# Kernel tuning notes

Measured on AMD Instinct MI355X. Metric: run time of the kernel, lower is better.

## Reference

```python
import jax, jax.numpy as jnp
import numpy as np

# Pyramid of RBS (Givens) gates on 6 wires: 15 gates, column-major diamond order.
PYRAMID_PAIRS = [(0,1),(1,2),(0,1),(2,3),(1,2),(3,4),(0,1),(2,3),(4,5),(1,2),(3,4),(0,1),(2,3),(1,2),(0,1)]


def setup_inputs() -> dict:
    key = jax.random.key(0)
    k1, k2, k3, k4, k5, k6 = jax.random.split(key, 6)
    B = 65536
    return {
        "inputs": jax.random.normal(k1, (B, 28, 28), dtype=jnp.float32),
        "dense_w": jax.random.normal(k2, (784, 6), dtype=jnp.float32) * 0.05,
        "dense_b": jax.random.normal(k3, (6,), dtype=jnp.float32) * 0.05,
        # module initializes quantum_weights to zeros; use small random angles for a
        # non-degenerate reference (zeros makes the pyramid the identity)
        "qweights": jax.random.normal(k4, (15,), dtype=jnp.float32) * 0.1,
        "out_w": jax.random.normal(k5, (6, 1), dtype=jnp.float32) * 0.5,
        "out_b": jax.random.normal(k6, (1,), dtype=jnp.float32) * 0.1,
    }


def _quantum_block(h, qweights):
    # vector_loader: encode normalized h into unary amplitudes (Hamming-weight-1 subspace)
    a = h / jnp.linalg.norm(h, axis=1, keepdims=True)  # [B, 6]; NaN if zero norm, sanitized below
    # pyramid_circuit: each RBS(theta) acts as a 2x2 Givens rotation on unary amplitudes
    for k, (i, j) in enumerate(PYRAMID_PAIRS):
        c, s = jnp.cos(qweights[k]), jnp.sin(qweights[k])
        ai, aj = a[:, i], a[:, j]
        a = a.at[:, i].set(c * ai + s * aj)
        a = a.at[:, j].set(-s * ai + c * aj)
    # <Z_i> on a unary state = 1 - 2 * P(qubit i = 1) = 1 - 2 * a_i^2
    z = 1.0 - 2.0 * a * a
    return jnp.where(jnp.isnan(z), jnp.zeros_like(z), z)


def reference(inputs, dense_w, dense_b, qweights, out_w, out_b):
    x = inputs.reshape(inputs.shape[0], -1)          # flatten [B, 784]
    h = x @ dense_w + dense_b                        # Dense(6, linear)
    z = _quantum_block(h, qweights)                  # batched statevector sim, [B, 6]
    return jax.nn.sigmoid(z @ out_w + out_b)         # Dense(1, sigmoid)
```

## Files before the change

### kernel.cpp

```cpp
#include <hip/hip_runtime.h>
#include <math.h>

#define TPB 256

__global__ __launch_bounds__(TPB) void hybrid_kernel(
    const float* __restrict__ inp,
    const float* __restrict__ dw,
    const float* __restrict__ db,
    const float* __restrict__ qw,
    const float* __restrict__ ow,
    const float* __restrict__ ob,
    float* __restrict__ out,
    int B)
{
    __shared__ float4 wT4[6 * 196];
    __shared__ float csc[15], css[15];
    __shared__ float sb[8], sw[8];
    __shared__ float sob;

    float* wT = (float*)wT4;
    const int tid = threadIdx.x;

    for (int i = tid; i < 4704; i += TPB) {
        int e = i / 6;
        int j = i - e * 6;
        wT[j * 784 + e] = dw[i];
    }
    if (tid < 15) { float q = qw[tid]; csc[tid] = cosf(q); css[tid] = sinf(q); }
    if (tid < 6)  { sb[tid] = db[tid]; sw[tid] = ow[tid]; }
    if (tid == 0) sob = ob[0];
    __syncthreads();

    const int lane = tid & 63;
    const int grp  = lane >> 4;
    const int gl   = lane & 15;
    const int row  = blockIdx.x * 16 + (tid >> 6) * 4 + grp;
    if (row >= B) return;

    const float4* x4 = (const float4*)(inp + (size_t)row * 784);

    float acc[6] = {0.f, 0.f, 0.f, 0.f, 0.f, 0.f};

    #pragma unroll 4
    for (int t = 0; t < 12; ++t) {
        const int idx4 = gl + 16 * t;
        const float4 xv = x4[idx4];
        #pragma unroll
        for (int j = 0; j < 6; ++j) {
            const float4 wv = wT4[j * 196 + idx4];
            acc[j] += xv.x * wv.x + xv.y * wv.y + xv.z * wv.z + xv.w * wv.w;
        }
    }
    if (gl < 4) {
        const int idx4 = 192 + gl;
        const float4 xv = x4[idx4];
        #pragma unroll
        for (int j = 0; j < 6; ++j) {
            const float4 wv = wT4[j * 196 + idx4];
            acc[j] += xv.x * wv.x + xv.y * wv.y + xv.z * wv.z + xv.w * wv.w;
        }
    }

    #pragma unroll
    for (int m = 1; m <= 8; m <<= 1) {
        #pragma unroll
        for (int j = 0; j < 6; ++j)
            acc[j] += __shfl_xor(acc[j], m, 64);
    }

    float a[6];
    float hh = 0.f;
    #pragma unroll
    for (int j = 0; j < 6; ++j) {
        a[j] = acc[j] + sb[j];
        hh += a[j] * a[j];
    }
    const float inv = rsqrtf(hh);
    #pragma unroll
    for (int j = 0; j < 6; ++j) a[j] *= inv;

    const int PI[15] = {0,1,0,2,1,3,0,2,4,1,3,0,2,1,0};
    #pragma unroll
    for (int k = 0; k < 15; ++k) {
        const int i = PI[k];
        const float c = csc[k], s = css[k];
        const float ai = a[i], aj = a[i + 1];
        a[i]     = c * ai + s * aj;
        a[i + 1] = c * aj - s * ai;
    }

    float v = sob;
    #pragma unroll
    for (int j = 0; j < 6; ++j) {
        float z = 1.f - 2.f * a[j] * a[j];
        z = isnan(z) ? 0.f : z;
        v += z * sw[j];
    }
    const float o = 1.f / (1.f + __expf(-v));

    if (gl == 0) out[row] = o;
}

extern "C" void kernel_launch(void* const* d_in, const int* in_sizes, int n_in,
                              void* d_out, int out_size, void* d_ws, size_t ws_size,
                              hipStream_t stream) {
    const float* inp = (const float*)d_in[0];
    const float* dw  = (const float*)d_in[1];
    const float* db  = (const float*)d_in[2];
    const float* qw  = (const float*)d_in[3];
    const float* ow  = (const float*)d_in[4];
    const float* ob  = (const float*)d_in[5];
    float* out = (float*)d_out;

    const int B = in_sizes[0] / 784;
    const int blocks = (B + 15) / 16;
    hybrid_kernel<<<blocks, TPB, 0, stream>>>(inp, dw, db, qw, ow, ob, out, B);
}
```

Before: 293.3 us.

## Process four rows per lane group to reuse LDS weights and amortize staging

Result: no change. 298.5 us (+1.8%).

```diff
diff --git a/kernel.cpp b/kernel.cpp
--- a/kernel.cpp
+++ b/kernel.cpp
@@ -34,71 +34,93 @@
     const int lane = tid & 63;
     const int grp  = lane >> 4;
     const int gl   = lane & 15;
-    const int row  = blockIdx.x * 16 + (tid >> 6) * 4 + grp;
-    if (row >= B) return;
+    const int wave = tid >> 6;
+    const int base = blockIdx.x * 64 + wave * 16 + grp * 4;
+    if (base >= B) return;
 
-    const float4* x4 = (const float4*)(inp + (size_t)row * 784);
+    const float4* x0 = (const float4*)(inp + (size_t)base * 784);
 
-    float acc[6] = {0.f, 0.f, 0.f, 0.f, 0.f, 0.f};
+    float acc[4][6];
+    #pragma unroll
+    for (int r = 0; r < 4; ++r)
+        #pragma unroll
+        for (int j = 0; j < 6; ++j) acc[r][j] = 0.f;
 
     #pragma unroll 4
     for (int t = 0; t < 12; ++t) {
         const int idx4 = gl + 16 * t;
-        const float4 xv = x4[idx4];
+        float4 xv[4];
+        #pragma unroll
+        for (int r = 0; r < 4; ++r) xv[r] = x0[r * 196 + idx4];
         #pragma unroll
         for (int j = 0; j < 6; ++j) {
             const float4 wv = wT4[j * 196 + idx4];
-            acc[j] += xv.x * wv.x + xv.y * wv.y + xv.z * wv.z + xv.w * wv.w;
+            #pragma unroll
+            for (int r = 0; r < 4; ++r)
+                acc[r][j] += xv[r].x * wv.x + xv[r].y * wv.y
+                           + xv[r].z * wv.z + xv[r].w * wv.w;
         }
     }
     if (gl < 4) {
         const int idx4 = 192 + gl;
-        const float4 xv = x4[idx4];
+        float4 xv[4];
+        #pragma unroll
+        for (int r = 0; r < 4; ++r) xv[r] = x0[r * 196 + idx4];
         #pragma unroll
         for (int j = 0; j < 6; ++j) {
             const float4 wv = wT4[j * 196 + idx4];
-            acc[j] += xv.x * wv.x + xv.y * wv.y + xv.z * wv.z + xv.w * wv.w;
+            #pragma unroll
+            for (int r = 0; r < 4; ++r)
+                acc[r][j] += xv[r].x * wv.x + xv[r].y * wv.y
+                           + xv[r].z * wv.z + xv[r].w * wv.w;
         }
     }
 
     #pragma unroll
     for (int m = 1; m <= 8; m <<= 1) {
         #pragma unroll
-        for (int j = 0; j < 6; ++j)
-            acc[j] += __shfl_xor(acc[j], m, 64);
+        for (int r = 0; r < 4; ++r)
+            #pragma unroll
+            for (int j = 0; j < 6; ++j)
+                acc[r][j] += __shfl_xor(acc[r][j], m, 64);
     }
 
-    float a[6];
-    float hh = 0.f;
+    const int PI[15] = {0,1,0,2,1,3,0,2,4,1,3,0,2,1,0};
+    float4 o4;
+    float* op = (float*)&o4;
     #pragma unroll
-    for (int j = 0; j < 6; ++j) {
-        a[j] = acc[j] + sb[j];
-        hh += a[j] * a[j];
-    }
-    const float inv = rsqrtf(hh);
-    #pragma unroll
-    for (int j = 0; j < 6; ++j) a[j] *= inv;
+    for (int r = 0; r < 4; ++r) {
+        float a[6];
+        float hh = 0.f;
+        #pragma unroll
+        for (int j = 0; j < 6; ++j) {
+            a[j] = acc[r][j] + sb[j];
+            hh += a[j] * a[j];
+        }
+        const float inv = rsqrtf(hh);
+        #pragma unroll
+        for (int j = 0; j < 6; ++j) a[j] *= inv;
 
-    const int PI[15] = {0,1,0,2,1,3,0,2,4,1,3,0,2,1,0};
-    #pragma unroll
-    for (int k = 0; k < 15; ++k) {
-        const int i = PI[k];
-        const float c = csc[k], s = css[k];
-        const float ai = a[i], aj = a[i + 1];
-        a[i]     = c * ai + s * aj;
-        a[i + 1] = c * aj - s * ai;
+        #pragma unroll
+        for (int k = 0; k < 15; ++k) {
+            const int i = PI[k];
+            const float c = csc[k], s = css[k];
+            const float ai = a[i], aj = a[i + 1];
+            a[i]     = c * ai + s * aj;
+            a[i + 1] = c * aj - s * ai;
+        }
+
+        float v = sob;
+        #pragma unroll
+        for (int j = 0; j < 6; ++j) {
+            float z = 1.f - 2.f * a[j] * a[j];
+            z = isnan(z) ? 0.f : z;
+            v += z * sw[j];
+        }
+        op[r] = 1.f / (1.f + __expf(-v));
     }
 
-    float v = sob;
-    #pragma unroll
-    for (int j = 0; j < 6; ++j) {
-        float z = 1.f - 2.f * a[j] * a[j];
-        z = isnan(z) ? 0.f : z;
-        v += z * sw[j];
-    }
-    const float o = 1.f / (1.f + __expf(-v));
-
-    if (gl == 0) out[row] = o;
+    if (gl == 0) *(float4*)(out + base) = o4;
 }
 
 extern "C" void kernel_launch(void* const* d_in, const int* in_sizes, int n_in,
@@ -113,6 +135,6 @@
     float* out = (float*)d_out;
 
     const int B = in_sizes[0] / 784;
-    const int blocks = (B + 15) / 16;
+    const int blocks = (B + 63) / 64;
     hybrid_kernel<<<blocks, TPB, 0, stream>>>(inp, dw, db, qw, ow, ob, out, B);
 }
```
